# Optimization experiments

Hardware: AMD Instinct MI355X
Metric: run time of the kernel (lower is better)

The kernel has to match this reference:

```python
import jax, jax.numpy as jnp
import numpy as np

N_USERS = 100000
N_ITEMS = 200000
D = 64
N_LAYERS = 2
UI_EDGES = 3200000
SOC_EDGES = 1600000
EPS = 1e-5  # torch LayerNorm default


def setup_inputs() -> dict:
    key = jax.random.key(0)
    ks = jax.random.split(key, 10)
    user_emb = jax.random.normal(ks[0], (N_USERS, D), jnp.float32)
    item_emb = jax.random.normal(ks[1], (N_ITEMS, D), jnp.float32)
    ui_src = jax.random.randint(ks[2], (UI_EDGES,), 0, N_USERS, jnp.int32)
    ui_dst = jax.random.randint(ks[3], (UI_EDGES,), 0, N_ITEMS, jnp.int32)
    ui_val = jax.random.uniform(ks[4], (UI_EDGES,), jnp.float32)
    soc_src = jax.random.randint(ks[5], (SOC_EDGES,), 0, N_USERS, jnp.int32)
    soc_dst = jax.random.randint(ks[6], (SOC_EDGES,), 0, N_USERS, jnp.int32)
    soc_val = jax.random.uniform(ks[7], (SOC_EDGES,), jnp.float32)
    # learned params: shared ui_transform / social_transform Linear per layer, 2*n_layers LayerNorms
    W_ui = jax.random.normal(ks[8], (N_LAYERS, D, D), jnp.float32) / np.sqrt(D).astype(np.float32)
    b_ui = jnp.zeros((N_LAYERS, D), jnp.float32)
    W_soc = jax.random.normal(ks[9], (N_LAYERS, D, D), jnp.float32) / np.sqrt(D).astype(np.float32)
    b_soc = jnp.zeros((N_LAYERS, D), jnp.float32)
    ln_g = jnp.ones((2 * N_LAYERS, D), jnp.float32)
    ln_b = jnp.zeros((2 * N_LAYERS, D), jnp.float32)
    return dict(user_emb=user_emb, item_emb=item_emb, ui_src=ui_src, ui_dst=ui_dst,
                ui_val=ui_val, soc_src=soc_src, soc_dst=soc_dst, soc_val=soc_val,
                W_ui=W_ui, b_ui=b_ui, W_soc=W_soc, b_soc=b_soc, ln_g=ln_g, ln_b=ln_b)


def _layernorm(x, g, b):
    m = jnp.mean(x, axis=-1, keepdims=True)
    v = jnp.var(x, axis=-1, keepdims=True)  # biased, as torch LayerNorm
    return (x - m) * jax.lax.rsqrt(v + EPS) * g + b


def _spmm(src, dst, val, x, n_rows):
    # out[r] = sum_{e: src[e]==r} val[e] * x[dst[e]]  (COO SpMM)
    return jax.ops.segment_sum(val[:, None] * x[dst], src, num_segments=n_rows)


def reference(user_emb, item_emb, ui_src, ui_dst, ui_val, soc_src, soc_dst, soc_val,
              W_ui, b_ui, W_soc, b_soc, ln_g, ln_b):
    n_users = user_emb.shape[0]
    n_items = item_emb.shape[0]
    ui_list = [user_emb]
    soc_list = [user_emb]
    u, it, s = user_emb, item_emb, user_emb
    for i in range(N_LAYERS):
        # user-item bipartite propagation (item_user = transpose of user_item)
        agg_u = _spmm(ui_src, ui_dst, ui_val, it, n_users) @ W_ui[i] + b_ui[i]
        agg_i = _spmm(ui_dst, ui_src, ui_val, u, n_items) @ W_ui[i] + b_ui[i]
        u = _layernorm(u + agg_u, ln_g[2 * i], ln_b[2 * i])
        it = _layernorm(it + agg_i, ln_g[2 * i + 1], ln_b[2 * i + 1])
        ui_list.append(u)
        # social propagation (shares layer_norms[2i] params with user branch)
        agg_s = _spmm(soc_src, soc_dst, soc_val, s, n_users) @ W_soc[i] + b_soc[i]
        s = _layernorm(s + agg_s, ln_g[2 * i], ln_b[2 * i])
        soc_list.append(s)
    # dropout is identity in eval/reference mode
    return (jnp.stack(ui_list), jnp.stack(soc_list), it)
```

## Files before the change

### kernel.cpp

```cpp
#include <hip/hip_runtime.h>
#include <stdint.h>

static constexpr int NU    = 100000;
static constexpr int NI    = 200000;
static constexpr int D     = 64;
static constexpr int E_UI  = 3200000;
static constexpr int E_SOC = 1600000;
static constexpr int CH    = 8192;
static constexpr int BROWS = 512;
#define EPS_LN 1e-5f

typedef __attribute__((ext_vector_type(8))) short bf16x8;
typedef __attribute__((ext_vector_type(4))) float f32x4;

__device__ __forceinline__ unsigned short f2b(float f) {
    unsigned u = __float_as_uint(f);
    u = (u + 0x7FFFu + ((u >> 16) & 1u)) >> 16;
    return (unsigned short)u;
}
__device__ __forceinline__ float b2fs(unsigned short h) {
    return __uint_as_float((unsigned)h << 16);
}
__device__ __forceinline__ float b2f_lo(unsigned u) { return __uint_as_float(u << 16); }
__device__ __forceinline__ float b2f_hi(unsigned u) { return __uint_as_float(u & 0xFFFF0000u); }

__global__ void __launch_bounds__(256) bin_count(
    const int* __restrict__ rows, int E, int nblk, int nb, int* __restrict__ cnt)
{
    __shared__ int hist[512];
    int b = blockIdx.x, t = threadIdx.x;
    for (int i = t; i < nb; i += 256) hist[i] = 0;
    __syncthreads();
    int e0 = b * CH, e1 = min(E, e0 + CH);
    for (int e = e0 + t; e < e1; e += 256)
        atomicAdd(&hist[rows[e] >> 9], 1);
    __syncthreads();
    for (int i = t; i < nb; i += 256) cnt[i * nblk + b] = hist[i];
}

__global__ void scan_partial(const int* __restrict__ cnt, int* __restrict__ bsum, int n)
{
    __shared__ int lds[256];
    int i = blockIdx.x * 256 + threadIdx.x;
    lds[threadIdx.x] = (i < n) ? cnt[i] : 0;
    __syncthreads();
    for (int off = 128; off > 0; off >>= 1) {
        if (threadIdx.x < off) lds[threadIdx.x] += lds[threadIdx.x + off];
        __syncthreads();
    }
    if (threadIdx.x == 0) bsum[blockIdx.x] = lds[0];
}

__global__ void scan_bsums(int* __restrict__ bsum, int nb)
{
    __shared__ int lds[1024];
    int t = threadIdx.x;
    int v = (t < nb) ? bsum[t] : 0;
    lds[t] = v;
    __syncthreads();
    for (int off = 1; off < 1024; off <<= 1) {
        int add = (t >= off) ? lds[t - off] : 0;
        __syncthreads();
        lds[t] += add;
        __syncthreads();
    }
    if (t < nb) bsum[t] = lds[t] - v;
}

__global__ void scan_out(const int* __restrict__ cnt, const int* __restrict__ bsum,
                         int* __restrict__ ofs, int n)
{
    __shared__ int lds[256];
    int i = blockIdx.x * 256 + threadIdx.x;
    int v = (i < n) ? cnt[i] : 0;
    lds[threadIdx.x] = v;
    __syncthreads();
    for (int off = 1; off < 256; off <<= 1) {
        int add = (threadIdx.x >= off) ? lds[threadIdx.x - off] : 0;
        __syncthreads();
        lds[threadIdx.x] += add;
        __syncthreads();
    }
    if (i < n) ofs[i] = bsum[blockIdx.x] + lds[threadIdx.x] - v;
}

__global__ void __launch_bounds__(256) bin_scatter(
    const int* __restrict__ rows, const int* __restrict__ idxs, const float* __restrict__ vals,
    int E, int nblk, const int* __restrict__ ofs, int nb, int2* __restrict__ binned)
{
    __shared__ int cur[512];
    int b = blockIdx.x, t = threadIdx.x;
    for (int i = t; i < nb; i += 256) cur[i] = ofs[i * nblk + b];
    __syncthreads();
    int e0 = b * CH, e1 = min(E, e0 + CH);
    for (int e = e0 + t; e < e1; e += 256) {
        int row = rows[e];
        int bucket = row >> 9;
        int slot = atomicAdd(&cur[bucket], 1);
        unsigned pack = ((unsigned)(row & 511) << 23) | (unsigned)idxs[e];
        binned[slot] = make_int2((int)pack, __float_as_int(vals[e]));
    }
}

__global__ void __launch_bounds__(512) fine_scatter(
    const int2* __restrict__ binned, const int* __restrict__ ofs, int nblk, int nb,
    int E, int nrows, int* __restrict__ rowptr, int2* __restrict__ rec)
{
    __shared__ int hist[512];
    __shared__ int cur[512];
    int b = blockIdx.x, t = threadIdx.x;
    int beg = ofs[b * nblk];
    int end = (b + 1 < nb) ? ofs[(b + 1) * nblk] : E;

    hist[t] = 0;
    __syncthreads();
    for (int j = beg + t; j < end; j += 512)
        atomicAdd(&hist[((unsigned)binned[j].x) >> 23], 1);
    __syncthreads();
    int v = hist[t];
    for (int off = 1; off < 512; off <<= 1) {
        int add = (t >= off) ? hist[t - off] : 0;
        __syncthreads();
        hist[t] += add;
        __syncthreads();
    }
    int excl = hist[t] - v;
    cur[t] = excl;
    int grow = b * BROWS + t;
    if (grow <= nrows) rowptr[grow] = beg + excl;
    __syncthreads();
    for (int j = beg + t; j < end; j += 512) {
        int2 eb = binned[j];
        unsigned p = (unsigned)eb.x;
        int rl  = (int)(p >> 23);
        int idx = (int)(p & 0x7FFFFFu);
        int c = atomicAdd(&cur[rl], 1);
        rec[beg + c] = make_int2(idx, eb.y);
    }
}

__global__ void copy0_kernel(const float4* __restrict__ src, float4* __restrict__ a,
                             float4* __restrict__ b, int n4)
{
    int i = blockIdx.x * blockDim.x + threadIdx.x;
    if (i < n4) { float4 v = src[i]; a[i] = v; b[i] = v; }
}

__global__ void f2b_kernel(const float4* __restrict__ src, ushort4* __restrict__ dst, int n4)
{
    int i = blockIdx.x * blockDim.x + threadIdx.x;
    if (i < n4) {
        float4 v = src[i];
        ushort4 h;
        h.x = f2b(v.x); h.y = f2b(v.y); h.z = f2b(v.z); h.w = f2b(v.w);
        dst[i] = h;
    }
}

struct TaskA {
    const unsigned short* gsrc;
    float* agg;
    const int* rowptr;
    const int2* recs;
    int nrows;
    int blk0;
};

__global__ void __launch_bounds__(256) spmm3(TaskA t0, TaskA t1, TaskA t2)
{
    TaskA t = (blockIdx.x >= (unsigned)t2.blk0) ? t2
            : (blockIdx.x >= (unsigned)t1.blk0) ? t1 : t0;
    int wid  = (blockIdx.x - t.blk0) * 4 + (threadIdx.x >> 6);
    int lane = threadIdx.x & 63;
    if (wid >= t.nrows) return;

    int g  = lane >> 3;
    int l8 = lane & 7;

    float a0[8], a1[8];
    #pragma unroll
    for (int m = 0; m < 8; ++m) { a0[m] = 0.f; a1[m] = 0.f; }

    int beg = t.rowptr[wid], end = t.rowptr[wid + 1];
    int j = beg + g;
    for (; j + 8 < end; j += 16) {
        int2 r0 = t.recs[j];
        int2 r1 = t.recs[j + 8];
        uint4 h0 = ((const uint4*)(t.gsrc + (size_t)r0.x * 64))[l8];
        uint4 h1 = ((const uint4*)(t.gsrc + (size_t)r1.x * 64))[l8];
        float w0 = __int_as_float(r0.y);
        float w1 = __int_as_float(r1.y);
        a0[0] += w0 * b2f_lo(h0.x); a0[1] += w0 * b2f_hi(h0.x);
        a0[2] += w0 * b2f_lo(h0.y); a0[3] += w0 * b2f_hi(h0.y);
        a0[4] += w0 * b2f_lo(h0.z); a0[5] += w0 * b2f_hi(h0.z);
        a0[6] += w0 * b2f_lo(h0.w); a0[7] += w0 * b2f_hi(h0.w);
        a1[0] += w1 * b2f_lo(h1.x); a1[1] += w1 * b2f_hi(h1.x);
        a1[2] += w1 * b2f_lo(h1.y); a1[3] += w1 * b2f_hi(h1.y);
        a1[4] += w1 * b2f_lo(h1.z); a1[5] += w1 * b2f_hi(h1.z);
        a1[6] += w1 * b2f_lo(h1.w); a1[7] += w1 * b2f_hi(h1.w);
    }
    for (; j < end; j += 8) {
        int2 r0 = t.recs[j];
        uint4 h0 = ((const uint4*)(t.gsrc + (size_t)r0.x * 64))[l8];
        float w0 = __int_as_float(r0.y);
        a0[0] += w0 * b2f_lo(h0.x); a0[1] += w0 * b2f_hi(h0.x);
        a0[2] += w0 * b2f_lo(h0.y); a0[3] += w0 * b2f_hi(h0.y);
        a0[4] += w0 * b2f_lo(h0.z); a0[5] += w0 * b2f_hi(h0.z);
        a0[6] += w0 * b2f_lo(h0.w); a0[7] += w0 * b2f_hi(h0.w);
    }
    float acc[8];
    #pragma unroll
    for (int m = 0; m < 8; ++m) acc[m] = a0[m] + a1[m];
    #pragma unroll
    for (int off = 8; off <= 32; off <<= 1)
        #pragma unroll
        for (int m = 0; m < 8; ++m)
            acc[m] += __shfl_xor(acc[m], off);

    if (g == 0) {
        float4 v0 = make_float4(acc[0], acc[1], acc[2], acc[3]);
        float4 v1 = make_float4(acc[4], acc[5], acc[6], acc[7]);
        float4* dst = (float4*)(t.agg + (size_t)wid * 64 + l8 * 8);
        dst[0] = v0;
        dst[1] = v1;
    }
}

struct TaskB {
    const float* agg;
    const float* xin;
    float* yout;
    unsigned short* youtb;
    const float* W;
    const float* bias;
    const float* gamma;
    const float* beta;
    int ntiles;
    int blk0;
    int nblk;
};

__device__ __forceinline__ void split_hi_lo(const f32x4 a, const f32x4 b,
                                            bf16x8& hi, bf16x8& lo)
{
    #pragma unroll
    for (int j = 0; j < 4; ++j) {
        unsigned short h = f2b(a[j]);
        hi[j] = (short)h;
        lo[j] = (short)f2b(a[j] - b2fs(h));
    }
    #pragma unroll
    for (int j = 0; j < 4; ++j) {
        unsigned short h = f2b(b[j]);
        hi[4 + j] = (short)h;
        lo[4 + j] = (short)f2b(b[j] - b2fs(h));
    }
}

__global__ void __launch_bounds__(256) gemmln3(TaskB t0, TaskB t1, TaskB t2)
{
    __shared__ float Wl[64 * 64];
    TaskB t = (blockIdx.x >= (unsigned)t2.blk0) ? t2
            : (blockIdx.x >= (unsigned)t1.blk0) ? t1 : t0;
    {
        const float4* W4 = (const float4*)t.W;
        float4* Wl4 = (float4*)Wl;
        for (int i = threadIdx.x; i < 1024; i += 256) Wl4[i] = W4[i];
    }
    __syncthreads();

    int wv   = threadIdx.x >> 6;
    int lane = threadIdx.x & 63;
    int g    = lane >> 4;
    int c    = lane & 15;

    bf16x8 Whi[2][4], Wlo[2][4];
    #pragma unroll
    for (int kt = 0; kt < 2; ++kt)
        #pragma unroll
        for (int nt = 0; nt < 4; ++nt) {
            #pragma unroll
            for (int j = 0; j < 8; ++j) {
                float w = Wl[(kt * 32 + 8 * g + j) * 64 + nt * 16 + c];
                unsigned short h = f2b(w);
                Whi[kt][nt][j] = (short)h;
                Wlo[kt][nt][j] = (short)f2b(w - b2fs(h));
            }
        }
    float bia[4], gam[4], bet[4];
    #pragma unroll
    for (int nt = 0; nt < 4; ++nt) {
        bia[nt] = t.bias[nt * 16 + c];
        gam[nt] = t.gamma[nt * 16 + c];
        bet[nt] = t.beta[nt * 16 + c];
    }

    int stride = t.nblk * 4;
    for (int tile = (blockIdx.x - t.blk0) * 4 + wv; tile < t.ntiles; tile += stride) {
        int rowbase = tile * 16;
        const float* arow = t.agg + (size_t)(rowbase + c) * 64 + 8 * g;
        f32x4 a00 = *(const f32x4*)(arow);
        f32x4 a01 = *(const f32x4*)(arow + 4);
        f32x4 a10 = *(const f32x4*)(arow + 32);
        f32x4 a11 = *(const f32x4*)(arow + 36);
        bf16x8 Ahi0, Alo0, Ahi1, Alo1;
        split_hi_lo(a00, a01, Ahi0, Alo0);
        split_hi_lo(a10, a11, Ahi1, Alo1);

        f32x4 acc[4];
        #pragma unroll
        for (int nt = 0; nt < 4; ++nt) {
            f32x4 z = {0.f, 0.f, 0.f, 0.f};
            z = __builtin_amdgcn_mfma_f32_16x16x32_bf16(Ahi0, Whi[0][nt], z, 0, 0, 0);
            z = __builtin_amdgcn_mfma_f32_16x16x32_bf16(Ahi1, Whi[1][nt], z, 0, 0, 0);
            z = __builtin_amdgcn_mfma_f32_16x16x32_bf16(Alo0, Whi[0][nt], z, 0, 0, 0);
            z = __builtin_amdgcn_mfma_f32_16x16x32_bf16(Alo1, Whi[1][nt], z, 0, 0, 0);
            z = __builtin_amdgcn_mfma_f32_16x16x32_bf16(Ahi0, Wlo[0][nt], z, 0, 0, 0);
            z = __builtin_amdgcn_mfma_f32_16x16x32_bf16(Ahi1, Wlo[1][nt], z, 0, 0, 0);
            acc[nt] = z;
        }

        float tv[4][4];
        #pragma unroll
        for (int reg = 0; reg < 4; ++reg) {
            int row = rowbase + 4 * g + reg;
            const float* xrow = t.xin + (size_t)row * 64 + c;
            #pragma unroll
            for (int nt = 0; nt < 4; ++nt)
                tv[nt][reg] = acc[nt][reg] + bia[nt] + xrow[nt * 16];
        }
        #pragma unroll
        for (int reg = 0; reg < 4; ++reg) {
            float s = tv[0][reg] + tv[1][reg] + tv[2][reg] + tv[3][reg];
            #pragma unroll
            for (int off = 1; off <= 8; off <<= 1) s += __shfl_xor(s, off);
            float mean = s * (1.0f / 64.0f);
            float q = 0.f;
            #pragma unroll
            for (int nt = 0; nt < 4; ++nt) {
                float dv = tv[nt][reg] - mean;
                q += dv * dv;
            }
            #pragma unroll
            for (int off = 1; off <= 8; off <<= 1) q += __shfl_xor(q, off);
            float rs = rsqrtf(q * (1.0f / 64.0f) + EPS_LN);
            int row = rowbase + 4 * g + reg;
            float* yrow = t.yout + (size_t)row * 64 + c;
            #pragma unroll
            for (int nt = 0; nt < 4; ++nt) {
                float y = (tv[nt][reg] - mean) * rs * gam[nt] + bet[nt];
                yrow[nt * 16] = y;
                if (t.youtb) t.youtb[(size_t)row * 64 + nt * 16 + c] = f2b(y);
            }
        }
    }
}

extern "C" void kernel_launch(void* const* d_in, const int* in_sizes, int n_in,
                              void* d_out, int out_size, void* d_ws, size_t ws_size,
                              hipStream_t stream)
{
    const float* user_emb = (const float*)d_in[0];
    const float* item_emb = (const float*)d_in[1];
    const int*   ui_src   = (const int*)d_in[2];
    const int*   ui_dst   = (const int*)d_in[3];
    const float* ui_val   = (const float*)d_in[4];
    const int*   soc_src  = (const int*)d_in[5];
    const int*   soc_dst  = (const int*)d_in[6];
    const float* soc_val  = (const float*)d_in[7];
    const float* W_ui     = (const float*)d_in[8];
    const float* b_ui     = (const float*)d_in[9];
    const float* W_soc    = (const float*)d_in[10];
    const float* b_soc    = (const float*)d_in[11];
    const float* ln_g     = (const float*)d_in[12];
    const float* ln_b     = (const float*)d_in[13];

    float* out     = (float*)d_out;
    float* out_ui  = out;
    float* out_soc = out + (size_t)3 * NU * D;
    float* out_it  = out + (size_t)6 * NU * D;

    const int NBU = (NU + BROWS - 1) / BROWS;
    const int NBI = (NI + BROWS - 1) / BROWS;
    const int BLK_UI  = (E_UI  + CH - 1) / CH;
    const int BLK_SOC = (E_SOC + CH - 1) / CH;

    char* p = (char*)d_ws;
    auto take = [&](size_t bytes) { char* r = p; p += (bytes + 255) & ~(size_t)255; return r; };
    int2* rec_us = (int2*)take((size_t)E_UI * 8);
    int2* rec_ud = (int2*)take((size_t)E_UI * 8);
    int2* rec_ss = (int2*)take((size_t)E_SOC * 8);
    int2* binned = (int2*)take((size_t)E_UI * 8);
    int*  rp_us  = (int*)take((size_t)(NU + 1) * 4);
    int*  rp_ud  = (int*)take((size_t)(NI + 1) * 4);
    int*  rp_ss  = (int*)take((size_t)(NU + 1) * 4);
    int*  cnt    = (int*)take((size_t)NBI * BLK_UI * 4);
    int*  ofs    = (int*)take((size_t)NBI * BLK_UI * 4);
    int*  bsum   = (int*)take(1024 * 4);
    unsigned short* u0b  = (unsigned short*)take((size_t)NU * D * 2);
    unsigned short* it0b = (unsigned short*)take((size_t)NI * D * 2);
    unsigned short* u1b  = (unsigned short*)take((size_t)NU * D * 2);
    unsigned short* s1b  = (unsigned short*)take((size_t)NU * D * 2);
    unsigned short* it1b = (unsigned short*)take((size_t)NI * D * 2);
    float* agg_i = (float*)take((size_t)NI * D * 4);
    float* agg_s = (float*)take((size_t)NU * D * 4);
    float* agg_u = (float*)binned;

    auto build_csr = [&](const int* rows, const int* idxs, const float* vals,
                         int E, int nblk, int nb, int nrows, int* rowptr, int2* rec) {
        bin_count<<<nblk, 256, 0, stream>>>(rows, E, nblk, nb, cnt);
        int n = nb * nblk;
        int sb = (n + 255) / 256;
        scan_partial<<<sb, 256, 0, stream>>>(cnt, bsum, n);
        scan_bsums<<<1, 1024, 0, stream>>>(bsum, sb);
        scan_out<<<sb, 256, 0, stream>>>(cnt, bsum, ofs, n);
        bin_scatter<<<nblk, 256, 0, stream>>>(rows, idxs, vals, E, nblk, ofs, nb, binned);
        fine_scatter<<<nb, 512, 0, stream>>>(binned, ofs, nblk, nb, E, nrows, rowptr, rec);
    };

    build_csr(ui_src,  ui_dst,  ui_val,  E_UI,  BLK_UI,  NBU, NU, rp_us, rec_us);
    build_csr(ui_dst,  ui_src,  ui_val,  E_UI,  BLK_UI,  NBI, NI, rp_ud, rec_ud);
    build_csr(soc_src, soc_dst, soc_val, E_SOC, BLK_SOC, NBU, NU, rp_ss, rec_ss);

    f2b_kernel<<<(NU * 16 + 255) / 256, 256, 0, stream>>>((const float4*)user_emb,
                                                          (ushort4*)u0b, NU * 16);
    f2b_kernel<<<(NI * 16 + 255) / 256, 256, 0, stream>>>((const float4*)item_emb,
                                                          (ushort4*)it0b, NI * 16);

    int n4 = NU * D / 4;
    copy0_kernel<<<(n4 + 255) / 256, 256, 0, stream>>>((const float4*)user_emb,
                                                       (float4*)out_ui, (float4*)out_soc, n4);

    const float* u0 = user_emb;
    float* u1 = out_ui + (size_t)NU * D;
    float* u2 = out_ui + (size_t)2 * NU * D;
    const float* s0 = user_emb;
    float* s1 = out_soc + (size_t)NU * D;
    float* s2 = out_soc + (size_t)2 * NU * D;

    int ublocks = (NU + 3) / 4;
    int iblocks = (NI + 3) / 4;
    int agrid   = iblocks + 2 * ublocks;

    const int NB_I = 1040, NB_U = 520, NB_S = 520;
    int bgrid = NB_I + NB_U + NB_S;
    const int TIL_I = NI / 16, TIL_U = NU / 16;

    {
        TaskA ai { u0b,  agg_i, rp_ud, rec_ud, NI, 0 };
        TaskA au { it0b, agg_u, rp_us, rec_us, NU, iblocks };
        TaskA as { u0b,  agg_s, rp_ss, rec_ss, NU, iblocks + ublocks };
        spmm3<<<agrid, 256, 0, stream>>>(ai, au, as);
    }
    {
        TaskB bi { agg_i, item_emb, out_it, it1b, W_ui + 0 * 4096, b_ui + 0 * 64,
                   ln_g + 1 * 64, ln_b + 1 * 64, TIL_I, 0, NB_I };
        TaskB bu { agg_u, u0, u1, u1b, W_ui + 0 * 4096, b_ui + 0 * 64,
                   ln_g + 0 * 64, ln_b + 0 * 64, TIL_U, NB_I, NB_U };
        TaskB bs { agg_s, s0, s1, s1b, W_soc + 0 * 4096, b_soc + 0 * 64,
                   ln_g + 0 * 64, ln_b + 0 * 64, TIL_U, NB_I + NB_U, NB_S };
        gemmln3<<<bgrid, 256, 0, stream>>>(bi, bu, bs);
    }

    {
        TaskA ai { u1b,  agg_i, rp_ud, rec_ud, NI, 0 };
        TaskA au { it1b, agg_u, rp_us, rec_us, NU, iblocks };
        TaskA as { s1b,  agg_s, rp_ss, rec_ss, NU, iblocks + ublocks };
        spmm3<<<agrid, 256, 0, stream>>>(ai, au, as);
    }
    {
        TaskB bi { agg_i, out_it, out_it, nullptr, W_ui + 1 * 4096, b_ui + 1 * 64,
                   ln_g + 3 * 64, ln_b + 3 * 64, TIL_I, 0, NB_I };
        TaskB bu { agg_u, u1, u2, nullptr, W_ui + 1 * 4096, b_ui + 1 * 64,
                   ln_g + 2 * 64, ln_b + 2 * 64, TIL_U, NB_I, NB_U };
        TaskB bs { agg_s, s1, s2, nullptr, W_soc + 1 * 4096, b_soc + 1 * 64,
                   ln_g + 2 * 64, ln_b + 2 * 64, TIL_U, NB_I + NB_U, NB_S };
        gemmln3<<<bgrid, 256, 0, stream>>>(bi, bu, bs);
    }
}
```

Measured before the change: 817.1 us.

## Apply linear transform before SpMM and fuse LayerNorm into the gather kernel

Uses the identity (A·x)·W = A·(x·W) to reorder each layer. A new MFMA kernel first writes x·W as bf16 tables. A fused SpMM kernel then gathers those tables and applies bias, residual and LayerNorm in one pass. This removes the fp32 aggregate buffers with their write and re-read, plus the separate bf16 conversion kernels. The cost is narrow scalar bf16 stores in the table kernel, and the gathered values are now rounded after the matmul instead of before it.

```diff
diff --git a/kernel.cpp b/kernel.cpp
--- a/kernel.cpp
+++ b/kernel.cpp
@@ -146,29 +146,106 @@
     if (i < n4) { float4 v = src[i]; a[i] = v; b[i] = v; }
 }
 
-__global__ void f2b_kernel(const float4* __restrict__ src, ushort4* __restrict__ dst, int n4)
-{
-    int i = blockIdx.x * blockDim.x + threadIdx.x;
-    if (i < n4) {
-        float4 v = src[i];
-        ushort4 h;
-        h.x = f2b(v.x); h.y = f2b(v.y); h.z = f2b(v.z); h.w = f2b(v.w);
-        dst[i] = h;
-    }
-}
-
-struct TaskA {
+struct TaskT {
+    const float* x;
+    unsigned short* tab;
+    const float* W;
+    int ntiles;
+    int blk0;
+    int nblk;
+};
+
+__device__ __forceinline__ void split_hi_lo(const f32x4 a, const f32x4 b,
+                                            bf16x8& hi, bf16x8& lo)
+{
+    #pragma unroll
+    for (int j = 0; j < 4; ++j) {
+        unsigned short h = f2b(a[j]);
+        hi[j] = (short)h;
+        lo[j] = (short)f2b(a[j] - b2fs(h));
+    }
+    #pragma unroll
+    for (int j = 0; j < 4; ++j) {
+        unsigned short h = f2b(b[j]);
+        hi[4 + j] = (short)h;
+        lo[4 + j] = (short)f2b(b[j] - b2fs(h));
+    }
+}
+
+__global__ void __launch_bounds__(256) btab3(TaskT t0, TaskT t1, TaskT t2)
+{
+    __shared__ float Wl[64 * 64];
+    TaskT t = (blockIdx.x >= (unsigned)t2.blk0) ? t2
+            : (blockIdx.x >= (unsigned)t1.blk0) ? t1 : t0;
+    {
+        const float4* W4 = (const float4*)t.W;
+        float4* Wl4 = (float4*)Wl;
+        for (int i = threadIdx.x; i < 1024; i += 256) Wl4[i] = W4[i];
+    }
+    __syncthreads();
+
+    int wv   = threadIdx.x >> 6;
+    int lane = threadIdx.x & 63;
+    int g    = lane >> 4;
+    int c    = lane & 15;
+
+    bf16x8 Whi[2][4], Wlo[2][4];
+    #pragma unroll
+    for (int kt = 0; kt < 2; ++kt)
+        #pragma unroll
+        for (int nt = 0; nt < 4; ++nt)
+            #pragma unroll
+            for (int j = 0; j < 8; ++j) {
+                float w = Wl[(kt * 32 + 8 * g + j) * 64 + nt * 16 + c];
+                unsigned short h = f2b(w);
+                Whi[kt][nt][j] = (short)h;
+                Wlo[kt][nt][j] = (short)f2b(w - b2fs(h));
+            }
+
+    int stride = t.nblk * 4;
+    for (int tile = (blockIdx.x - t.blk0) * 4 + wv; tile < t.ntiles; tile += stride) {
+        int rowbase = tile * 16;
+        const float* arow = t.x + (size_t)(rowbase + c) * 64 + 8 * g;
+        f32x4 a00 = *(const f32x4*)(arow);
+        f32x4 a01 = *(const f32x4*)(arow + 4);
+        f32x4 a10 = *(const f32x4*)(arow + 32);
+        f32x4 a11 = *(const f32x4*)(arow + 36);
+        bf16x8 Ahi0, Alo0, Ahi1, Alo1;
+        split_hi_lo(a00, a01, Ahi0, Alo0);
+        split_hi_lo(a10, a11, Ahi1, Alo1);
+
+        #pragma unroll
+        for (int nt = 0; nt < 4; ++nt) {
+            f32x4 z = {0.f, 0.f, 0.f, 0.f};
+            z = __builtin_amdgcn_mfma_f32_16x16x32_bf16(Ahi0, Whi[0][nt], z, 0, 0, 0);
+            z = __builtin_amdgcn_mfma_f32_16x16x32_bf16(Ahi1, Whi[1][nt], z, 0, 0, 0);
+            z = __builtin_amdgcn_mfma_f32_16x16x32_bf16(Alo0, Whi[0][nt], z, 0, 0, 0);
+            z = __builtin_amdgcn_mfma_f32_16x16x32_bf16(Alo1, Whi[1][nt], z, 0, 0, 0);
+            z = __builtin_amdgcn_mfma_f32_16x16x32_bf16(Ahi0, Wlo[0][nt], z, 0, 0, 0);
+            z = __builtin_amdgcn_mfma_f32_16x16x32_bf16(Ahi1, Wlo[1][nt], z, 0, 0, 0);
+            #pragma unroll
+            for (int reg = 0; reg < 4; ++reg)
+                t.tab[(size_t)(rowbase + 4 * g + reg) * 64 + nt * 16 + c] = f2b(z[reg]);
+        }
+    }
+}
+
+struct TaskS {
     const unsigned short* gsrc;
-    float* agg;
+    const float* xin;
+    float* yout;
     const int* rowptr;
     const int2* recs;
+    const float* bias;
+    const float* gamma;
+    const float* beta;
     int nrows;
     int blk0;
 };
 
-__global__ void __launch_bounds__(256) spmm3(TaskA t0, TaskA t1, TaskA t2)
-{
-    TaskA t = (blockIdx.x >= (unsigned)t2.blk0) ? t2
+__global__ void __launch_bounds__(256) spmmln3(TaskS t0, TaskS t1, TaskS t2)
+{
+    TaskS t = (blockIdx.x >= (unsigned)t2.blk0) ? t2
             : (blockIdx.x >= (unsigned)t1.blk0) ? t1 : t0;
     int wid  = (blockIdx.x - t.blk0) * 4 + (threadIdx.x >> 6);
     int lane = threadIdx.x & 63;
@@ -217,142 +294,46 @@
         for (int m = 0; m < 8; ++m)
             acc[m] += __shfl_xor(acc[m], off);
 
+    const float4* xi = (const float4*)(t.xin + (size_t)wid * 64 + 8 * l8);
+    const float4* bi = (const float4*)(t.bias + 8 * l8);
+    float4 x0 = xi[0], x1 = xi[1];
+    float4 bb0 = bi[0], bb1 = bi[1];
+    float tv[8];
+    tv[0] = x0.x + acc[0] + bb0.x; tv[1] = x0.y + acc[1] + bb0.y;
+    tv[2] = x0.z + acc[2] + bb0.z; tv[3] = x0.w + acc[3] + bb0.w;
+    tv[4] = x1.x + acc[4] + bb1.x; tv[5] = x1.y + acc[5] + bb1.y;
+    tv[6] = x1.z + acc[6] + bb1.z; tv[7] = x1.w + acc[7] + bb1.w;
+
+    float s = 0.f;
+    #pragma unroll
+    for (int m = 0; m < 8; ++m) s += tv[m];
+    #pragma unroll
+    for (int off = 1; off <= 4; off <<= 1) s += __shfl_xor(s, off);
+    float mean = s * (1.0f / 64.0f);
+    float q = 0.f;
+    #pragma unroll
+    for (int m = 0; m < 8; ++m) { float dv = tv[m] - mean; q += dv * dv; }
+    #pragma unroll
+    for (int off = 1; off <= 4; off <<= 1) q += __shfl_xor(q, off);
+    float rs = rsqrtf(q * (1.0f / 64.0f) + EPS_LN);
+
     if (g == 0) {
-        float4 v0 = make_float4(acc[0], acc[1], acc[2], acc[3]);
-        float4 v1 = make_float4(acc[4], acc[5], acc[6], acc[7]);
-        float4* dst = (float4*)(t.agg + (size_t)wid * 64 + l8 * 8);
-        dst[0] = v0;
-        dst[1] = v1;
-    }
-}
-
-struct TaskB {
-    const float* agg;
-    const float* xin;
-    float* yout;
-    unsigned short* youtb;
-    const float* W;
-    const float* bias;
-    const float* gamma;
-    const float* beta;
-    int ntiles;
-    int blk0;
-    int nblk;
-};
-
-__device__ __forceinline__ void split_hi_lo(const f32x4 a, const f32x4 b,
-                                            bf16x8& hi, bf16x8& lo)
-{
-    #pragma unroll
-    for (int j = 0; j < 4; ++j) {
-        unsigned short h = f2b(a[j]);
-        hi[j] = (short)h;
-        lo[j] = (short)f2b(a[j] - b2fs(h));
-    }
-    #pragma unroll
-    for (int j = 0; j < 4; ++j) {
-        unsigned short h = f2b(b[j]);
-        hi[4 + j] = (short)h;
-        lo[4 + j] = (short)f2b(b[j] - b2fs(h));
-    }
-}
-
-__global__ void __launch_bounds__(256) gemmln3(TaskB t0, TaskB t1, TaskB t2)
-{
-    __shared__ float Wl[64 * 64];
-    TaskB t = (blockIdx.x >= (unsigned)t2.blk0) ? t2
-            : (blockIdx.x >= (unsigned)t1.blk0) ? t1 : t0;
-    {
-        const float4* W4 = (const float4*)t.W;
-        float4* Wl4 = (float4*)Wl;
-        for (int i = threadIdx.x; i < 1024; i += 256) Wl4[i] = W4[i];
-    }
-    __syncthreads();
-
-    int wv   = threadIdx.x >> 6;
-    int lane = threadIdx.x & 63;
-    int g    = lane >> 4;
-    int c    = lane & 15;
-
-    bf16x8 Whi[2][4], Wlo[2][4];
-    #pragma unroll
-    for (int kt = 0; kt < 2; ++kt)
-        #pragma unroll
-        for (int nt = 0; nt < 4; ++nt) {
-            #pragma unroll
-            for (int j = 0; j < 8; ++j) {
-                float w = Wl[(kt * 32 + 8 * g + j) * 64 + nt * 16 + c];
-                unsigned short h = f2b(w);
-                Whi[kt][nt][j] = (short)h;
-                Wlo[kt][nt][j] = (short)f2b(w - b2fs(h));
-            }
-        }
-    float bia[4], gam[4], bet[4];
-    #pragma unroll
-    for (int nt = 0; nt < 4; ++nt) {
-        bia[nt] = t.bias[nt * 16 + c];
-        gam[nt] = t.gamma[nt * 16 + c];
-        bet[nt] = t.beta[nt * 16 + c];
-    }
-
-    int stride = t.nblk * 4;
-    for (int tile = (blockIdx.x - t.blk0) * 4 + wv; tile < t.ntiles; tile += stride) {
-        int rowbase = tile * 16;
-        const float* arow = t.agg + (size_t)(rowbase + c) * 64 + 8 * g;
-        f32x4 a00 = *(const f32x4*)(arow);
-        f32x4 a01 = *(const f32x4*)(arow + 4);
-        f32x4 a10 = *(const f32x4*)(arow + 32);
-        f32x4 a11 = *(const f32x4*)(arow + 36);
-        bf16x8 Ahi0, Alo0, Ahi1, Alo1;
-        split_hi_lo(a00, a01, Ahi0, Alo0);
-        split_hi_lo(a10, a11, Ahi1, Alo1);
-
-        f32x4 acc[4];
-        #pragma unroll
-        for (int nt = 0; nt < 4; ++nt) {
-            f32x4 z = {0.f, 0.f, 0.f, 0.f};
-            z = __builtin_amdgcn_mfma_f32_16x16x32_bf16(Ahi0, Whi[0][nt], z, 0, 0, 0);
-            z = __builtin_amdgcn_mfma_f32_16x16x32_bf16(Ahi1, Whi[1][nt], z, 0, 0, 0);
-            z = __builtin_amdgcn_mfma_f32_16x16x32_bf16(Alo0, Whi[0][nt], z, 0, 0, 0);
-            z = __builtin_amdgcn_mfma_f32_16x16x32_bf16(Alo1, Whi[1][nt], z, 0, 0, 0);
-            z = __builtin_amdgcn_mfma_f32_16x16x32_bf16(Ahi0, Wlo[0][nt], z, 0, 0, 0);
-            z = __builtin_amdgcn_mfma_f32_16x16x32_bf16(Ahi1, Wlo[1][nt], z, 0, 0, 0);
-            acc[nt] = z;
-        }
-
-        float tv[4][4];
-        #pragma unroll
-        for (int reg = 0; reg < 4; ++reg) {
-            int row = rowbase + 4 * g + reg;
-            const float* xrow = t.xin + (size_t)row * 64 + c;
-            #pragma unroll
-            for (int nt = 0; nt < 4; ++nt)
-                tv[nt][reg] = acc[nt][reg] + bia[nt] + xrow[nt * 16];
-        }
-        #pragma unroll
-        for (int reg = 0; reg < 4; ++reg) {
-            float s = tv[0][reg] + tv[1][reg] + tv[2][reg] + tv[3][reg];
-            #pragma unroll
-            for (int off = 1; off <= 8; off <<= 1) s += __shfl_xor(s, off);
-            float mean = s * (1.0f / 64.0f);
-            float q = 0.f;
-            #pragma unroll
-            for (int nt = 0; nt < 4; ++nt) {
-                float dv = tv[nt][reg] - mean;
-                q += dv * dv;
-            }
-            #pragma unroll
-            for (int off = 1; off <= 8; off <<= 1) q += __shfl_xor(q, off);
-            float rs = rsqrtf(q * (1.0f / 64.0f) + EPS_LN);
-            int row = rowbase + 4 * g + reg;
-            float* yrow = t.yout + (size_t)row * 64 + c;
-            #pragma unroll
-            for (int nt = 0; nt < 4; ++nt) {
-                float y = (tv[nt][reg] - mean) * rs * gam[nt] + bet[nt];
-                yrow[nt * 16] = y;
-                if (t.youtb) t.youtb[(size_t)row * 64 + nt * 16 + c] = f2b(y);
-            }
-        }
+        const float4* ga = (const float4*)(t.gamma + 8 * l8);
+        const float4* be = (const float4*)(t.beta + 8 * l8);
+        float4 g0 = ga[0], g1 = ga[1];
+        float4 e0 = be[0], e1 = be[1];
+        float4 y0, y1;
+        y0.x = (tv[0] - mean) * rs * g0.x + e0.x;
+        y0.y = (tv[1] - mean) * rs * g0.y + e0.y;
+        y0.z = (tv[2] - mean) * rs * g0.z + e0.z;
+        y0.w = (tv[3] - mean) * rs * g0.w + e0.w;
+        y1.x = (tv[4] - mean) * rs * g1.x + e1.x;
+        y1.y = (tv[5] - mean) * rs * g1.y + e1.y;
+        y1.z = (tv[6] - mean) * rs * g1.z + e1.z;
+        y1.w = (tv[7] - mean) * rs * g1.w + e1.w;
+        float4* yo = (float4*)(t.yout + (size_t)wid * 64 + 8 * l8);
+        yo[0] = y0;
+        yo[1] = y1;
     }
 }
 
@@ -397,14 +378,9 @@
     int*  cnt    = (int*)take((size_t)NBI * BLK_UI * 4);
     int*  ofs    = (int*)take((size_t)NBI * BLK_UI * 4);
     int*  bsum   = (int*)take(1024 * 4);
-    unsigned short* u0b  = (unsigned short*)take((size_t)NU * D * 2);
-    unsigned short* it0b = (unsigned short*)take((size_t)NI * D * 2);
-    unsigned short* u1b  = (unsigned short*)take((size_t)NU * D * 2);
-    unsigned short* s1b  = (unsigned short*)take((size_t)NU * D * 2);
-    unsigned short* it1b = (unsigned short*)take((size_t)NI * D * 2);
-    float* agg_i = (float*)take((size_t)NI * D * 4);
-    float* agg_s = (float*)take((size_t)NU * D * 4);
-    float* agg_u = (float*)binned;
+    unsigned short* twi = (unsigned short*)take((size_t)NU * D * 2);
+    unsigned short* tws = (unsigned short*)take((size_t)NU * D * 2);
+    unsigned short* twu = (unsigned short*)binned;
 
     auto build_csr = [&](const int* rows, const int* idxs, const float* vals,
                          int E, int nblk, int nb, int nrows, int* rowptr, int2* rec) {
@@ -422,11 +398,6 @@
     build_csr(ui_dst,  ui_src,  ui_val,  E_UI,  BLK_UI,  NBI, NI, rp_ud, rec_ud);
     build_csr(soc_src, soc_dst, soc_val, E_SOC, BLK_SOC, NBU, NU, rp_ss, rec_ss);
 
-    f2b_kernel<<<(NU * 16 + 255) / 256, 256, 0, stream>>>((const float4*)user_emb,
-                                                          (ushort4*)u0b, NU * 16);
-    f2b_kernel<<<(NI * 16 + 255) / 256, 256, 0, stream>>>((const float4*)item_emb,
-                                                          (ushort4*)it0b, NI * 16);
-
     int n4 = NU * D / 4;
     copy0_kernel<<<(n4 + 255) / 256, 256, 0, stream>>>((const float4*)user_emb,
                                                        (float4*)out_ui, (float4*)out_soc, n4);
@@ -442,39 +413,39 @@
     int iblocks = (NI + 3) / 4;
     int agrid   = iblocks + 2 * ublocks;
 
-    const int NB_I = 1040, NB_U = 520, NB_S = 520;
-    int bgrid = NB_I + NB_U + NB_S;
+    const int TB_I = 1040, TB_U = 520, TB_S = 520;
+    int tgrid = TB_I + TB_U + TB_S;
     const int TIL_I = NI / 16, TIL_U = NU / 16;
 
     {
-        TaskA ai { u0b,  agg_i, rp_ud, rec_ud, NI, 0 };
-        TaskA au { it0b, agg_u, rp_us, rec_us, NU, iblocks };
-        TaskA as { u0b,  agg_s, rp_ss, rec_ss, NU, iblocks + ublocks };
-        spmm3<<<agrid, 256, 0, stream>>>(ai, au, as);
+        TaskT ta { item_emb, twu, W_ui + 0 * 4096, TIL_I, 0, TB_I };
+        TaskT tb { u0,       twi, W_ui + 0 * 4096, TIL_U, TB_I, TB_U };
+        TaskT tc { u0,       tws, W_soc + 0 * 4096, TIL_U, TB_I + TB_U, TB_S };
+        btab3<<<tgrid, 256, 0, stream>>>(ta, tb, tc);
     }
     {
-        TaskB bi { agg_i, item_emb, out_it, it1b, W_ui + 0 * 4096, b_ui + 0 * 64,
-                   ln_g + 1 * 64, ln_b + 1 * 64, TIL_I, 0, NB_I };
-        TaskB bu { agg_u, u0, u1, u1b, W_ui + 0 * 4096, b_ui + 0 * 64,
-                   ln_g + 0 * 64, ln_b + 0 * 64, TIL_U, NB_I, NB_U };
-        TaskB bs { agg_s, s0, s1, s1b, W_soc + 0 * 4096, b_soc + 0 * 64,
-                   ln_g + 0 * 64, ln_b + 0 * 64, TIL_U, NB_I + NB_U, NB_S };
-        gemmln3<<<bgrid, 256, 0, stream>>>(bi, bu, bs);
+        TaskS si { twi, item_emb, out_it, rp_ud, rec_ud, b_ui + 0 * 64,
+                   ln_g + 1 * 64, ln_b + 1 * 64, NI, 0 };
+        TaskS su { twu, u0, u1, rp_us, rec_us, b_ui + 0 * 64,
+                   ln_g + 0 * 64, ln_b + 0 * 64, NU, iblocks };
+        TaskS ss { tws, s0, s1, rp_ss, rec_ss, b_soc + 0 * 64,
+                   ln_g + 0 * 64, ln_b + 0 * 64, NU, iblocks + ublocks };
+        spmmln3<<<agrid, 256, 0, stream>>>(si, su, ss);
     }
 
     {
-        TaskA ai { u1b,  agg_i, rp_ud, rec_ud, NI, 0 };
-        TaskA au { it1b, agg_u, rp_us, rec_us, NU, iblocks };
-        TaskA as { s1b,  agg_s, rp_ss, rec_ss, NU, iblocks + ublocks };
-        spmm3<<<agrid, 256, 0, stream>>>(ai, au, as);
+        TaskT ta { out_it, twu, W_ui + 1 * 4096, TIL_I, 0, TB_I };
+        TaskT tb { u1,     twi, W_ui + 1 * 4096, TIL_U, TB_I, TB_U };
+        TaskT tc { s1,     tws, W_soc + 1 * 4096, TIL_U, TB_I + TB_U, TB_S };
+        btab3<<<tgrid, 256, 0, stream>>>(ta, tb, tc);
     }
     {
-        TaskB bi { agg_i, out_it, out_it, nullptr, W_ui + 1 * 4096, b_ui + 1 * 64,
-                   ln_g + 3 * 64, ln_b + 3 * 64, TIL_I, 0, NB_I };
-        TaskB bu { agg_u, u1, u2, nullptr, W_ui + 1 * 4096, b_ui + 1 * 64,
-                   ln_g + 2 * 64, ln_b + 2 * 64, TIL_U, NB_I, NB_U };
-        TaskB bs { agg_s, s1, s2, nullptr, W_soc + 1 * 4096, b_soc + 1 * 64,
-                   ln_g + 2 * 64, ln_b + 2 * 64, TIL_U, NB_I + NB_U, NB_S };
-        gemmln3<<<bgrid, 256, 0, stream>>>(bi, bu, bs);
-    }
-}
+        TaskS si { twi, out_it, out_it, rp_ud, rec_ud, b_ui + 1 * 64,
+                   ln_g + 3 * 64, ln_b + 3 * 64, NI, 0 };
+        TaskS su { twu, u1, u2, rp_us, rec_us, b_ui + 1 * 64,
+                   ln_g + 2 * 64, ln_b + 2 * 64, NU, iblocks };
+        TaskS ss { tws, s1, s2, rp_ss, rec_ss, b_soc + 1 * 64,
+                   ln_g + 2 * 64, ln_b + 2 * 64, NU, iblocks + ublocks };
+        spmmln3<<<agrid, 256, 0, stream>>>(si, su, ss);
+    }
+}
```

Result: no change. 812.6 us (-0.6%).
